# Optimization experiments

Hardware: AMD Instinct MI355X
Metric: run time of the kernel (lower is better)

Reference implementation:

```python
import jax, jax.numpy as jnp
import numpy as np

N_SUP, D = 4096, 128
N_CLASSES, SHOTS = 128, 32          # balanced episode: N_SUP = N_CLASSES * SHOTS
N_QUERY = 65536
N_BOOT = 8                          # num_bootstrap_samples


def setup_inputs() -> dict:
    key = jax.random.key(0)
    k_sup, k_q, k_boot = jax.random.split(key, 3)
    support_set_repr = jax.random.normal(k_sup, (N_SUP, D), dtype=jnp.float32)
    # balanced, sorted labels: class c owns contiguous block [c*SHOTS, (c+1)*SHOTS)
    support_labels = (jnp.arange(N_SUP, dtype=jnp.int32) // SHOTS).astype(jnp.int32)
    query_set_repr = jax.random.normal(k_q, (N_QUERY, D), dtype=jnp.float32)
    # externalized torch.randint(0, num_samples, (B, num_samples)) per class
    bootstrap_indices = jax.random.randint(
        k_boot, (N_BOOT, N_CLASSES, SHOTS), 0, SHOTS, dtype=jnp.int32)
    return {
        "support_set_repr": support_set_repr,
        "support_labels": support_labels,
        "query_set_repr": query_set_repr,
        "bootstrap_indices": bootstrap_indices,
    }


def reference(support_set_repr, support_labels, query_set_repr, bootstrap_indices):
    B, C, S = bootstrap_indices.shape
    d = support_set_repr.shape[-1]
    # labels are sorted & balanced (arange // SHOTS), so per-class gather == reshape
    class_repr = support_set_repr.reshape(C, S, d)              # [C, S, D]
    # fused bootstrap gather: [B, C, S, D]
    boot = jnp.take_along_axis(class_repr[None], bootstrap_indices[..., None], axis=2)
    protos = boot.mean(axis=2)                                   # [B, C, D]
    # cdist(q, protos, p=2) via ||q||^2 + ||p||^2 - 2 q.p
    q2 = jnp.sum(query_set_repr * query_set_repr, axis=-1)       # [NQ]
    p2 = jnp.sum(protos * protos, axis=-1)                       # [B, C]
    qp = jnp.einsum('qd,bcd->bqc', query_set_repr, protos)       # [B, NQ, C]
    d2 = q2[None, :, None] + p2[:, None, :] - 2.0 * qp
    dists = jnp.sqrt(jnp.maximum(d2, 0.0))                       # [B, NQ, C]
    # logits = mean over bootstraps of -dists
    return -dists.mean(axis=0)                                   # [NQ, C]
```

## Files before the change

### kernel.cpp

```cpp
#include <hip/hip_runtime.h>
#include <hip/hip_bf16.h>


#define DIM   128
#define NCLS  128
#define SHOTS 32
#define NB    8
#define NQ    65536

using short8 = __attribute__((ext_vector_type(8))) short;
using f32x4  = __attribute__((ext_vector_type(4))) float;

__device__ __forceinline__ unsigned short f2bf(float x) {
  union { float f; unsigned u; } v; v.f = x;
  unsigned r = v.u + 0x7fffu + ((v.u >> 16) & 1u);
  return (unsigned short)(r >> 16);
}

__device__ __forceinline__ short8 pack8_bf16(float4 a, float4 b) {
  __hip_bfloat162 p0 = __float22bfloat162_rn(make_float2(a.x, a.y));
  __hip_bfloat162 p1 = __float22bfloat162_rn(make_float2(a.z, a.w));
  __hip_bfloat162 p2 = __float22bfloat162_rn(make_float2(b.x, b.y));
  __hip_bfloat162 p3 = __float22bfloat162_rn(make_float2(b.z, b.w));
  union { __hip_bfloat162 h[4]; short8 s; } u;
  u.h[0] = p0; u.h[1] = p1; u.h[2] = p2; u.h[3] = p3;
  return u.s;
}

__device__ __forceinline__ float fast_sqrt(float x) {
#if __has_builtin(__builtin_amdgcn_sqrtf)
  return __builtin_amdgcn_sqrtf(x);
#else
  return sqrtf(x);
#endif
}

__global__ __launch_bounds__(128) void proto_kernel(
    const float* __restrict__ sup, const int* __restrict__ bidx,
    unsigned short* __restrict__ pfrag, float* __restrict__ p2) {
  int bc = blockIdx.x;
  int c  = bc & (NCLS - 1);
  int d  = threadIdx.x;
  __shared__ int   sidx[SHOTS];
  __shared__ float wsum[2];
  if (d < SHOTS) sidx[d] = bidx[bc * SHOTS + d];
  __syncthreads();
  float acc = 0.f;
  const float* base = sup + c * SHOTS * DIM + d;
  #pragma unroll
  for (int s = 0; s < SHOTS; ++s) acc += base[sidx[s] * DIM];
  float proto = acc * (1.0f / 32.0f);

  int b     = bc >> 7;
  int ct    = c >> 4, l15c = c & 15;
  int kiter = d >> 5, quad = (d >> 3) & 3, j = d & 7;
  int lane  = l15c + (quad << 4);
  int slot  = (b * 8 + ct) * 4 + kiter;
  pfrag[slot * 512 + lane * 8 + j] = f2bf(proto * -0.03125f);

  float sq = proto * proto;
  #pragma unroll
  for (int off = 32; off > 0; off >>= 1) sq += __shfl_down(sq, off, 64);
  if ((d & 63) == 0) wsum[d >> 6] = sq;
  __syncthreads();
  if (d == 0) p2[bc] = (wsum[0] + wsum[1]) * (1.0f / 64.0f);
}

#define SLOT_STRIDE 520

__global__ __launch_bounds__(256) void dist_kernel(
    const float* __restrict__ q, const uint4* __restrict__ pfrag,
    const float* __restrict__ p2, float* __restrict__ out) {
  int tid  = threadIdx.x;
  int w    = tid >> 6, lane = tid & 63;
  int l15  = lane & 15, quad = lane >> 4;
  int q0   = blockIdx.x << 5;

  __shared__ unsigned short aflds[8 * SLOT_STRIDE];
  __shared__ float q2s[32];

  {
    int rloc  = w * 8 + (lane >> 3);
    int chunk = lane & 7;
    const float* src = q + (size_t)(q0 + rloc) * DIM + chunk * 16;
    float4 x0 = *reinterpret_cast<const float4*>(src);
    float4 x1 = *reinterpret_cast<const float4*>(src + 4);
    float4 x2 = *reinterpret_cast<const float4*>(src + 8);
    float4 x3 = *reinterpret_cast<const float4*>(src + 12);
    float s = x0.x*x0.x + x0.y*x0.y + x0.z*x0.z + x0.w*x0.w
            + x1.x*x1.x + x1.y*x1.y + x1.z*x1.z + x1.w*x1.w
            + x2.x*x2.x + x2.y*x2.y + x2.z*x2.z + x2.w*x2.w
            + x3.x*x3.x + x3.y*x3.y + x3.z*x3.z + x3.w*x3.w;
    s += __shfl_down(s, 4, 8);
    s += __shfl_down(s, 2, 8);
    s += __shfl_down(s, 1, 8);
    if (chunk == 0) q2s[rloc] = s;

    int mt = rloc >> 4, m = rloc & 15, i = chunk >> 1, h = chunk & 1;
    unsigned short* base = &aflds[(mt * 4 + i) * SLOT_STRIDE];
    *reinterpret_cast<short8*>(&base[((h * 2 + 0) * 16 + m) * 8]) = pack8_bf16(x0, x1);
    *reinterpret_cast<short8*>(&base[((h * 2 + 1) * 16 + m) * 8]) = pack8_bf16(x2, x3);
  }
  __syncthreads();

  short8 af[2][4];
  #pragma unroll
  for (int mt = 0; mt < 2; ++mt)
    #pragma unroll
    for (int k = 0; k < 4; ++k)
      af[mt][k] = *reinterpret_cast<const short8*>(
          &aflds[(mt * 4 + k) * SLOT_STRIDE + lane * 8]);

  f32x4 q2r[2];
  #pragma unroll
  for (int mt = 0; mt < 2; ++mt)
    #pragma unroll
    for (int r = 0; r < 4; ++r)
      q2r[mt][r] = q2s[mt * 16 + quad * 4 + r] * (1.0f / 64.0f);

  float p2v[NB][2];
  #pragma unroll
  for (int b = 0; b < NB; ++b)
    #pragma unroll
    for (int jj = 0; jj < 2; ++jj)
      p2v[b][jj] = p2[b * NCLS + (w * 2 + jj) * 16 + l15];

  f32x4 oacc[2][2];
  #pragma unroll
  for (int i = 0; i < 2; ++i)
    #pragma unroll
    for (int jj = 0; jj < 2; ++jj)
      oacc[i][jj] = (f32x4){0.f, 0.f, 0.f, 0.f};

  uint4 bufX[8], bufY[8];

  #define LOAD_B(BUF, B)                                                      \
    {                                                                         \
      _Pragma("unroll")                                                       \
      for (int jj = 0; jj < 2; ++jj) {                                        \
        int ct = w * 2 + jj;                                                  \
        const uint4* bp = pfrag + (size_t)(((B) * 8 + ct) * 4) * 64 + lane;   \
        _Pragma("unroll")                                                     \
        for (int k = 0; k < 4; ++k) BUF[jj * 4 + k] = bp[k * 64];             \
      }                                                                       \
    }

  #define COMPUTE_B(BUF, B)                                                   \
    {                                                                         \
      _Pragma("unroll")                                                       \
      for (int jj = 0; jj < 2; ++jj) {                                        \
        f32x4 qp0, qp1;                                                       \
        _Pragma("unroll")                                                     \
        for (int r = 0; r < 4; ++r) {                                         \
          qp0[r] = q2r[0][r] + p2v[B][jj];                                    \
          qp1[r] = q2r[1][r] + p2v[B][jj];                                    \
        }                                                                     \
        _Pragma("unroll")                                                     \
        for (int k = 0; k < 4; ++k) {                                         \
          short8 bfk = __builtin_bit_cast(short8, BUF[jj * 4 + k]);           \
          qp0 = __builtin_amdgcn_mfma_f32_16x16x32_bf16(af[0][k], bfk, qp0, 0, 0, 0); \
          qp1 = __builtin_amdgcn_mfma_f32_16x16x32_bf16(af[1][k], bfk, qp1, 0, 0, 0); \
        }                                                                     \
        _Pragma("unroll")                                                     \
        for (int r = 0; r < 4; ++r) {                                         \
          oacc[0][jj][r] += fast_sqrt(fmaxf(qp0[r], 0.0f));                   \
          oacc[1][jj][r] += fast_sqrt(fmaxf(qp1[r], 0.0f));                   \
        }                                                                     \
      }                                                                       \
    }

  LOAD_B(bufX, 0)
  #pragma unroll 1
  for (int i = 0; i < NB; i += 2) {
    LOAD_B(bufY, i + 1)
    COMPUTE_B(bufX, i)
    LOAD_B(bufX, (i + 2) & (NB - 1))
    COMPUTE_B(bufY, i + 1)
  }
  #undef LOAD_B
  #undef COMPUTE_B

  #pragma unroll
  for (int mt2 = 0; mt2 < 2; ++mt2)
    #pragma unroll
    for (int jj = 0; jj < 2; ++jj) {
      int col = (w * 2 + jj) * 16 + l15;
      #pragma unroll
      for (int r = 0; r < 4; ++r) {
        int row = q0 + mt2 * 16 + quad * 4 + r;
        out[(size_t)row * NCLS + col] = -oacc[mt2][jj][r];
      }
    }
}

extern "C" void kernel_launch(void* const* d_in, const int* in_sizes, int n_in,
                              void* d_out, int out_size, void* d_ws, size_t ws_size,
                              hipStream_t stream) {
  const float* sup   = (const float*)d_in[0];
  const float* query = (const float*)d_in[2];
  const int*   bidx  = (const int*)d_in[3];
  float* out = (float*)d_out;

  unsigned short* pfrag = (unsigned short*)d_ws;
  float* p2 = (float*)((char*)d_ws + (size_t)NB * NCLS * DIM * 2);

  proto_kernel<<<NB * NCLS, 128, 0, stream>>>(sup, bidx, pfrag, p2);
  dist_kernel<<<NQ / 32, 256, 0, stream>>>(query, (const uint4*)pfrag, p2, out);
}
```

Baseline: 112.9 us.

## Double query rows per block to reuse prototype fragments across four M-tiles

Each block now handles 64 queries instead of 32, so every loaded prototype B-fragment feeds four MFMA M-tiles instead of two. This halves prototype fragment traffic per query and halves the grid size. The software pipeline is reorganized into 16 half-groups, with per-group p2 loads replacing the preloaded p2 array. In exchange, each thread holds more A fragments and accumulators, which raises register pressure, and there are fewer blocks to spread across CUs.

```diff
diff --git a/kernel.cpp b/kernel.cpp
--- a/kernel.cpp
+++ b/kernel.cpp
@@ -74,121 +74,111 @@
   int tid  = threadIdx.x;
   int w    = tid >> 6, lane = tid & 63;
   int l15  = lane & 15, quad = lane >> 4;
-  int q0   = blockIdx.x << 5;
+  int q0   = blockIdx.x << 6;
 
-  __shared__ unsigned short aflds[8 * SLOT_STRIDE];
-  __shared__ float q2s[32];
+  __shared__ unsigned short aflds[16 * SLOT_STRIDE];
+  __shared__ float q2s[64];
 
   {
-    int rloc  = w * 8 + (lane >> 3);
-    int chunk = lane & 7;
-    const float* src = q + (size_t)(q0 + rloc) * DIM + chunk * 16;
-    float4 x0 = *reinterpret_cast<const float4*>(src);
-    float4 x1 = *reinterpret_cast<const float4*>(src + 4);
-    float4 x2 = *reinterpret_cast<const float4*>(src + 8);
-    float4 x3 = *reinterpret_cast<const float4*>(src + 12);
-    float s = x0.x*x0.x + x0.y*x0.y + x0.z*x0.z + x0.w*x0.w
-            + x1.x*x1.x + x1.y*x1.y + x1.z*x1.z + x1.w*x1.w
-            + x2.x*x2.x + x2.y*x2.y + x2.z*x2.z + x2.w*x2.w
-            + x3.x*x3.x + x3.y*x3.y + x3.z*x3.z + x3.w*x3.w;
-    s += __shfl_down(s, 4, 8);
-    s += __shfl_down(s, 2, 8);
-    s += __shfl_down(s, 1, 8);
-    if (chunk == 0) q2s[rloc] = s;
+    int rloc = tid >> 2;
+    int i    = tid & 3;
+    const float* src = q + (size_t)(q0 + rloc) * DIM + i * 32;
+    float4 x[8];
+    #pragma unroll
+    for (int v = 0; v < 8; ++v) x[v] = *reinterpret_cast<const float4*>(src + v * 4);
+    float s = 0.f;
+    #pragma unroll
+    for (int v = 0; v < 8; ++v)
+      s += x[v].x*x[v].x + x[v].y*x[v].y + x[v].z*x[v].z + x[v].w*x[v].w;
+    s += __shfl_down(s, 2, 4);
+    s += __shfl_down(s, 1, 4);
+    if (i == 0) q2s[rloc] = s;
 
-    int mt = rloc >> 4, m = rloc & 15, i = chunk >> 1, h = chunk & 1;
+    int mt = rloc >> 4, m = rloc & 15;
     unsigned short* base = &aflds[(mt * 4 + i) * SLOT_STRIDE];
-    *reinterpret_cast<short8*>(&base[((h * 2 + 0) * 16 + m) * 8]) = pack8_bf16(x0, x1);
-    *reinterpret_cast<short8*>(&base[((h * 2 + 1) * 16 + m) * 8]) = pack8_bf16(x2, x3);
+    #pragma unroll
+    for (int qd = 0; qd < 4; ++qd)
+      *reinterpret_cast<short8*>(&base[((qd << 4) + m) * 8]) =
+          pack8_bf16(x[qd * 2], x[qd * 2 + 1]);
   }
   __syncthreads();
 
-  short8 af[2][4];
+  short8 af[4][4];
   #pragma unroll
-  for (int mt = 0; mt < 2; ++mt)
+  for (int mt = 0; mt < 4; ++mt)
     #pragma unroll
     for (int k = 0; k < 4; ++k)
       af[mt][k] = *reinterpret_cast<const short8*>(
           &aflds[(mt * 4 + k) * SLOT_STRIDE + lane * 8]);
 
-  f32x4 q2r[2];
+  f32x4 q2r[4];
   #pragma unroll
-  for (int mt = 0; mt < 2; ++mt)
+  for (int mt = 0; mt < 4; ++mt)
     #pragma unroll
     for (int r = 0; r < 4; ++r)
       q2r[mt][r] = q2s[mt * 16 + quad * 4 + r] * (1.0f / 64.0f);
 
-  float p2v[NB][2];
+  f32x4 oacc[4][2];
   #pragma unroll
-  for (int b = 0; b < NB; ++b)
+  for (int mt = 0; mt < 4; ++mt)
     #pragma unroll
     for (int jj = 0; jj < 2; ++jj)
-      p2v[b][jj] = p2[b * NCLS + (w * 2 + jj) * 16 + l15];
+      oacc[mt][jj] = (f32x4){0.f, 0.f, 0.f, 0.f};
 
-  f32x4 oacc[2][2];
-  #pragma unroll
-  for (int i = 0; i < 2; ++i)
-    #pragma unroll
-    for (int jj = 0; jj < 2; ++jj)
-      oacc[i][jj] = (f32x4){0.f, 0.f, 0.f, 0.f};
+  uint4 bufX[4], bufY[4];
+  float p2X, p2Y;
 
-  uint4 bufX[8], bufY[8];
-
-  #define LOAD_B(BUF, B)                                                      \
+  #define LOAD_G(BUF, P2G, G)                                                 \
     {                                                                         \
+      int b_ = (G) >> 1, ct_ = w * 2 + ((G) & 1);                             \
+      const uint4* bp = pfrag + (size_t)((b_ * 8 + ct_) * 4) * 64 + lane;     \
       _Pragma("unroll")                                                       \
-      for (int jj = 0; jj < 2; ++jj) {                                        \
-        int ct = w * 2 + jj;                                                  \
-        const uint4* bp = pfrag + (size_t)(((B) * 8 + ct) * 4) * 64 + lane;   \
-        _Pragma("unroll")                                                     \
-        for (int k = 0; k < 4; ++k) BUF[jj * 4 + k] = bp[k * 64];             \
-      }                                                                       \
+      for (int k = 0; k < 4; ++k) BUF[k] = bp[k * 64];                        \
+      P2G = p2[b_ * NCLS + ct_ * 16 + l15];                                   \
     }
 
-  #define COMPUTE_B(BUF, B)                                                   \
+  #define COMPUTE_G(BUF, P2G, G)                                              \
     {                                                                         \
+      int jj_ = (G) & 1;                                                      \
+      f32x4 qp[4];                                                            \
       _Pragma("unroll")                                                       \
-      for (int jj = 0; jj < 2; ++jj) {                                        \
-        f32x4 qp0, qp1;                                                       \
+      for (int mt = 0; mt < 4; ++mt)                                          \
         _Pragma("unroll")                                                     \
-        for (int r = 0; r < 4; ++r) {                                         \
-          qp0[r] = q2r[0][r] + p2v[B][jj];                                    \
-          qp1[r] = q2r[1][r] + p2v[B][jj];                                    \
-        }                                                                     \
+        for (int r = 0; r < 4; ++r) qp[mt][r] = q2r[mt][r] + P2G;             \
+      _Pragma("unroll")                                                       \
+      for (int k = 0; k < 4; ++k) {                                           \
+        short8 bfk = __builtin_bit_cast(short8, BUF[k]);                      \
         _Pragma("unroll")                                                     \
-        for (int k = 0; k < 4; ++k) {                                         \
-          short8 bfk = __builtin_bit_cast(short8, BUF[jj * 4 + k]);           \
-          qp0 = __builtin_amdgcn_mfma_f32_16x16x32_bf16(af[0][k], bfk, qp0, 0, 0, 0); \
-          qp1 = __builtin_amdgcn_mfma_f32_16x16x32_bf16(af[1][k], bfk, qp1, 0, 0, 0); \
-        }                                                                     \
+        for (int mt = 0; mt < 4; ++mt)                                        \
+          qp[mt] = __builtin_amdgcn_mfma_f32_16x16x32_bf16(af[mt][k], bfk, qp[mt], 0, 0, 0); \
+      }                                                                       \
+      _Pragma("unroll")                                                       \
+      for (int mt = 0; mt < 4; ++mt)                                          \
         _Pragma("unroll")                                                     \
-        for (int r = 0; r < 4; ++r) {                                         \
-          oacc[0][jj][r] += fast_sqrt(fmaxf(qp0[r], 0.0f));                   \
-          oacc[1][jj][r] += fast_sqrt(fmaxf(qp1[r], 0.0f));                   \
-        }                                                                     \
-      }                                                                       \
+        for (int r = 0; r < 4; ++r)                                           \
+          oacc[mt][jj_][r] += fast_sqrt(fmaxf(qp[mt][r], 0.0f));              \
     }
 
-  LOAD_B(bufX, 0)
+  LOAD_G(bufX, p2X, 0)
   #pragma unroll 1
-  for (int i = 0; i < NB; i += 2) {
-    LOAD_B(bufY, i + 1)
-    COMPUTE_B(bufX, i)
-    LOAD_B(bufX, (i + 2) & (NB - 1))
-    COMPUTE_B(bufY, i + 1)
+  for (int g = 0; g < 16; g += 2) {
+    LOAD_G(bufY, p2Y, g + 1)
+    COMPUTE_G(bufX, p2X, g)
+    LOAD_G(bufX, p2X, (g + 2) & 15)
+    COMPUTE_G(bufY, p2Y, g + 1)
   }
-  #undef LOAD_B
-  #undef COMPUTE_B
+  #undef LOAD_G
+  #undef COMPUTE_G
 
   #pragma unroll
-  for (int mt2 = 0; mt2 < 2; ++mt2)
+  for (int mt = 0; mt < 4; ++mt)
     #pragma unroll
     for (int jj = 0; jj < 2; ++jj) {
       int col = (w * 2 + jj) * 16 + l15;
       #pragma unroll
       for (int r = 0; r < 4; ++r) {
-        int row = q0 + mt2 * 16 + quad * 4 + r;
-        out[(size_t)row * NCLS + col] = -oacc[mt2][jj][r];
+        int row = q0 + mt * 16 + quad * 4 + r;
+        out[(size_t)row * NCLS + col] = -oacc[mt][jj][r];
       }
     }
 }
@@ -205,5 +195,5 @@
   float* p2 = (float*)((char*)d_ws + (size_t)NB * NCLS * DIM * 2);
 
   proto_kernel<<<NB * NCLS, 128, 0, stream>>>(sup, bidx, pfrag, p2);
-  dist_kernel<<<NQ / 32, 256, 0, stream>>>(query, (const uint4*)pfrag, p2, out);
+  dist_kernel<<<NQ / 64, 256, 0, stream>>>(query, (const uint4*)pfrag, p2, out);
 }
```

Measured after the change: 117.2 us. +3.8%, slower.
